# Kernel tuning notes

Hardware: AMD Instinct MI355X
Metric: run time of the kernel (lower is better)

The kernel has to match this reference:

```python
import jax, jax.numpy as jnp
import numpy as np

P, M, DG, F, H, DH = 2000, 150, 2000, 256, 4, 64
N1, N2 = P + M, P + DG          # adj1 nodes (patient+med), adj2 nodes (patient+diag)
E1, E2, EGP, EGM = 137600, 256000, 64000, 4800
GNN_LAYERS = 2
SA_HID = 128


def setup_inputs() -> dict:
    key = jax.random.key(0)
    ks = jax.random.split(key, 32)
    ri = lambda k, n, hi: jax.random.randint(k, (n,), 0, hi, dtype=jnp.int32)
    rn = lambda k, shape, scale: (jax.random.normal(k, shape, dtype=jnp.float32) * scale)
    inp = {
        'adj1_rows': ri(ks[0], E1, N1), 'adj1_cols': ri(ks[1], E1, N1),
        'adj1_vals': jax.random.uniform(ks[2], (E1,), dtype=jnp.float32),
        'adj2_rows': ri(ks[3], E2, N2), 'adj2_cols': ri(ks[4], E2, N2),
        'adj2_vals': jax.random.uniform(ks[5], (E2,), dtype=jnp.float32),
        'g0_src': ri(ks[6], EGP, P), 'g0_dst': ri(ks[7], EGP, P),
        'g1_src': ri(ks[8], EGP, P), 'g1_dst': ri(ks[9], EGP, P),
        'g2_src': ri(ks[10], EGM, M), 'g2_dst': ri(ks[11], EGM, M),
        'g3_src': ri(ks[12], EGM, M), 'g3_dst': ri(ks[13], EGM, M),
        'keepRate': 1,
        # learned parameters (xavier-ish scales)
        'pEmbed': rn(ks[14], (P, F), 0.05),
        'mEmbed': rn(ks[15], (M, F), 0.05),
        'dEmbed': rn(ks[16], (DG, F), 0.05),
        'gat_W': rn(ks[17], (4, F, H * DH), (2.0 / (F + H * DH)) ** 0.5),
        'gat_al': rn(ks[18], (4, H, DH), 0.1),
        'gat_ar': rn(ks[19], (4, H, DH), 0.1),
        'gat_b': jnp.zeros((4, H * DH), dtype=jnp.float32),
        'sa_W1': rn(ks[20], (H * DH, SA_HID), (2.0 / (H * DH + SA_HID)) ** 0.5),
        'sa_b1': jnp.zeros((SA_HID,), dtype=jnp.float32),
        'sa_W2': rn(ks[21], (SA_HID, 1), 0.1),
        'out_W': rn(ks[22], (2 * F, M), (2.0 / (2 * F + M)) ** 0.5),
        'out_b': jnp.zeros((M,), dtype=jnp.float32),
    }
    return inp


def _spmm(rows, cols, vals, x, n):
    # sparse adj @ x via gather + segment_sum
    return jax.ops.segment_sum(vals[:, None] * x[cols], rows, num_segments=n)


def _seg_softmax(e, seg, n):
    m = jax.ops.segment_max(e, seg, num_segments=n)          # [n, H]
    ex = jnp.exp(e - m[seg])
    s = jax.ops.segment_sum(ex, seg, num_segments=n)
    return ex / (s[seg] + 1e-9)


def _gat(h, W, al, ar, b, src, dst, n):
    # DGL GATConv, feat/attn dropout = 0, negative_slope = 0.2, activation = elu
    feat = (h @ W).reshape(n, H, DH)                          # [n, H, DH]
    el = (feat * al[None]).sum(-1)                            # [n, H]
    er = (feat * ar[None]).sum(-1)
    e = jax.nn.leaky_relu(el[src] + er[dst], negative_slope=0.2)  # [E, H]
    alpha = _seg_softmax(e, dst, n)                           # softmax over in-edges per dst
    out = jax.ops.segment_sum(alpha[:, :, None] * feat[src], dst, num_segments=n)
    out = out + b.reshape(1, H, DH)
    return jax.nn.elu(out).reshape(n, H * DH)


def _sem_att(z, W1, b1, W2):
    # z: [N, K, F]; shared projection; beta over K meta-paths
    w = (jnp.tanh(z @ W1 + b1) @ W2).mean(0)                  # [K, 1]
    beta = jax.nn.softmax(w, axis=0)                          # [K, 1]
    return (beta[None] * z).sum(1)                            # [N, F]


def reference(adj1_rows, adj1_cols, adj1_vals, adj2_rows, adj2_cols, adj2_vals,
              g0_src, g0_dst, g1_src, g1_dst, g2_src, g2_dst, g3_src, g3_dst,
              keepRate, pEmbed, mEmbed, dEmbed, gat_W, gat_al, gat_ar, gat_b,
              sa_W1, sa_b1, sa_W2, out_W, out_b):
    embeds1 = jnp.concatenate([pEmbed, mEmbed], axis=0)       # [N1, F]
    embeds2 = jnp.concatenate([pEmbed, dEmbed], axis=0)       # [N2, F]
    lat1, lat2 = embeds1, embeds2
    acc1 = jnp.zeros_like(embeds1)
    acc2 = jnp.zeros_like(embeds2)
    for _ in range(GNN_LAYERS):
        lat1 = jax.nn.leaky_relu(_spmm(adj1_rows, adj1_cols, adj1_vals, lat1, N1), negative_slope=0.5)
        lat2 = jax.nn.leaky_relu(_spmm(adj2_rows, adj2_cols, adj2_vals, lat2, N2), negative_slope=0.5)
        acc1 = acc1 + lat1
        acc2 = acc2 + lat2
    p1, m_gcn = acc1[:P], acc1[P:]
    p2, d_gcn = acc2[:P], acc2[P:]

    e0 = _gat(p1, gat_W[0], gat_al[0], gat_ar[0], gat_b[0], g0_src, g0_dst, P)
    e1 = _gat(p2, gat_W[1], gat_al[1], gat_ar[1], gat_b[1], g1_src, g1_dst, P)
    e2 = _gat(m_gcn, gat_W[2], gat_al[2], gat_ar[2], gat_b[2], g2_src, g2_dst, M)
    e3 = _gat(m_gcn, gat_W[3], gat_al[3], gat_ar[3], gat_b[3], g3_src, g3_dst, M)

    patient = _sem_att(jnp.stack([e0, e1], axis=1), sa_W1, sa_b1, sa_W2)  # [P, F]
    med = _sem_att(jnp.stack([e2, e3], axis=1), sa_W1, sa_b1, sa_W2)      # [M, F]

    # broadcasted pairwise concat -> ReLU -> Linear -> sum over pairing axis
    pm = jnp.concatenate([
        jnp.broadcast_to(patient[:, None, :], (P, M, F)),
        jnp.broadcast_to(med[None, :, :], (P, M, F)),
    ], axis=-1).reshape(P * M, 2 * F)
    simi = (jax.nn.relu(pm) @ out_W + out_b).reshape(P, M, M)
    simi_pm = simi.sum(axis=1)                                # [P, M]
    return (simi_pm, d_gcn, med, m_gcn, patient)
```

## Files before the change

### kernel.cpp

```cpp
#include <hip/hip_runtime.h>
#include <cmath>
#include <cstdint>

constexpr int P  = 2000, M = 150, DG = 2000, F = 256, H = 4, DH = 64;
constexpr int N1 = P + M;
constexpr int N2 = P + DG;
constexpr int E1 = 137600, E2 = 256000, EGP = 64000, EGM = 4800;
constexpr int SA_HID = 128;

constexpr int HO1 = E1, HO2 = E1 + E2, HO3 = HO2 + EGP, HO4 = HO3 + EGP,
              HO5 = HO4 + EGM, HOE = HO5 + EGM;

constexpr int CAP_A = 160;
constexpr int CAP_G = 96;
constexpr int OVF_CAP = 4096;

constexpr int CPAD = 16;

__global__ __launch_bounds__(256) void k_build(
    const int* __restrict__ a1r, const int* __restrict__ a1c, const float* __restrict__ a1v,
    const int* __restrict__ a2r, const int* __restrict__ a2c, const float* __restrict__ a2v,
    const int* __restrict__ d0, const int* __restrict__ s0,
    const int* __restrict__ d1, const int* __restrict__ s1,
    const int* __restrict__ d2, const int* __restrict__ s2,
    const int* __restrict__ d3, const int* __restrict__ s3,
    int* cur1, uint2* ell1, int* cur2, uint2* ell2,
    int* cu0, unsigned* eg0, int* cu1, unsigned* eg1,
    int* cu2, unsigned* eg2, int* cu3, unsigned* eg3,
    int* __restrict__ ovf_n, int4* __restrict__ ovf) {
  int tid = blockIdx.x * 256 + threadIdx.x;
  int T = gridDim.x * 256;
  int seg[4], row[4]; unsigned p0[4], p1[4];
#pragma unroll
  for (int u = 0; u < 4; ++u) {
    int i = tid + u * T;
    seg[u] = -1;
    if (i < HOE) {
      if (i < HO1)      { seg[u] = 0; row[u] = a1r[i]; p0[u] = (unsigned)a1c[i]; p1[u] = __float_as_uint(a1v[i]); }
      else if (i < HO2) { int j = i - HO1; seg[u] = 1; row[u] = a2r[j]; p0[u] = (unsigned)a2c[j]; p1[u] = __float_as_uint(a2v[j]); }
      else if (i < HO3) { int j = i - HO2; seg[u] = 2; row[u] = d0[j]; p0[u] = (unsigned)s0[j]; }
      else if (i < HO4) { int j = i - HO3; seg[u] = 3; row[u] = d1[j]; p0[u] = (unsigned)s1[j]; }
      else if (i < HO5) { int j = i - HO4; seg[u] = 4; row[u] = d2[j]; p0[u] = (unsigned)s2[j]; }
      else              { int j = i - HO5; seg[u] = 5; row[u] = d3[j]; p0[u] = (unsigned)s3[j]; }
    }
  }
#pragma unroll
  for (int u = 0; u < 4; ++u) {
    int r = row[u];
    switch (seg[u]) {
      case 0: { int slot = atomicAdd(&cur1[(size_t)r * CPAD], 1);
        if (slot < CAP_A) ell1[(size_t)r * CAP_A + slot] = make_uint2(p0[u], p1[u]);
        else { int o = atomicAdd(&ovf_n[0], 1); if (o < OVF_CAP) ovf[0 * OVF_CAP + o] = make_int4(r, (int)p0[u], (int)p1[u], 0); } } break;
      case 1: { int slot = atomicAdd(&cur2[(size_t)r * CPAD], 1);
        if (slot < CAP_A) ell2[(size_t)r * CAP_A + slot] = make_uint2(p0[u], p1[u]);
        else { int o = atomicAdd(&ovf_n[1], 1); if (o < OVF_CAP) ovf[1 * OVF_CAP + o] = make_int4(r, (int)p0[u], (int)p1[u], 0); } } break;
      case 2: { int slot = atomicAdd(&cu0[(size_t)r * CPAD], 1);
        if (slot < CAP_G) eg0[(size_t)r * CAP_G + slot] = p0[u];
        else { int o = atomicAdd(&ovf_n[2], 1); if (o < OVF_CAP) ovf[2 * OVF_CAP + o] = make_int4(r, (int)p0[u], 0, 0); } } break;
      case 3: { int slot = atomicAdd(&cu1[(size_t)r * CPAD], 1);
        if (slot < CAP_G) eg1[(size_t)r * CAP_G + slot] = p0[u];
        else { int o = atomicAdd(&ovf_n[3], 1); if (o < OVF_CAP) ovf[3 * OVF_CAP + o] = make_int4(r, (int)p0[u], 0, 0); } } break;
      case 4: { int slot = atomicAdd(&cu2[(size_t)r * CPAD], 1);
        if (slot < CAP_G) eg2[(size_t)r * CAP_G + slot] = p0[u];
        else { int o = atomicAdd(&ovf_n[4], 1); if (o < OVF_CAP) ovf[4 * OVF_CAP + o] = make_int4(r, (int)p0[u], 0, 0); } } break;
      case 5: { int slot = atomicAdd(&cu3[(size_t)r * CPAD], 1);
        if (slot < CAP_G) eg3[(size_t)r * CAP_G + slot] = p0[u];
        else { int o = atomicAdd(&ovf_n[5], 1); if (o < OVF_CAP) ovf[5 * OVF_CAP + o] = make_int4(r, (int)p0[u], 0, 0); } } break;
      default: break;
    }
  }
}

template<int LAYER>
__global__ __launch_bounds__(256) void k_spmm(
    const int* __restrict__ cur1, const uint2* __restrict__ ell1,
    const int* __restrict__ cur2, const uint2* __restrict__ ell2,
    const int* __restrict__ ovf_n, const int4* __restrict__ ovf,
    const float* __restrict__ pE, const float* __restrict__ mE, const float* __restrict__ dE,
    float* __restrict__ lat1, float* __restrict__ lat2,
    float* __restrict__ acc1, float* __restrict__ acc2,
    float* __restrict__ out_mgcn, float* __restrict__ out_dgcn) {
  int gw = (blockIdx.x * 256 + threadIdx.x) >> 6;
  if (gw >= N1 + N2) return;
  int lane = threadIdx.x & 63;
  bool g2 = gw >= N1;
  int row = g2 ? gw - N1 : gw;
  const uint2* pe = (g2 ? ell2 : ell1) + (size_t)row * CAP_A;
  const float* latin = g2 ? lat2 : lat1;
  const float* tailE = g2 ? dE : mE;
  int deg = (g2 ? cur2 : cur1)[(size_t)row * CPAD];
  int dn = deg < CAP_A ? deg : CAP_A;
  int fo = lane << 2;
  float4 s = {0.f, 0.f, 0.f, 0.f};
  auto fetch = [&](int c) -> float4 {
    const float* b;
    if (LAYER == 1) b = (c < P) ? (pE + (size_t)c * F) : (tailE + (size_t)(c - P) * F);
    else            b = latin + (size_t)c * F;
    return *(const float4*)(b + fo);
  };
  int i = 0;
  for (; i + 8 <= dn; i += 8) {
    uint2 m[8]; float4 a[8];
#pragma unroll
    for (int u = 0; u < 8; ++u) m[u] = pe[i + u];
#pragma unroll
    for (int u = 0; u < 8; ++u) a[u] = fetch((int)m[u].x);
#pragma unroll
    for (int u = 0; u < 8; ++u) {
      float v = __uint_as_float(m[u].y);
      s.x += v * a[u].x; s.y += v * a[u].y; s.z += v * a[u].z; s.w += v * a[u].w;
    }
  }
  for (; i + 4 <= dn; i += 4) {
    uint2 m0 = pe[i], m1 = pe[i + 1], m2 = pe[i + 2], m3 = pe[i + 3];
    float v0 = __uint_as_float(m0.y), v1 = __uint_as_float(m1.y),
          v2 = __uint_as_float(m2.y), v3 = __uint_as_float(m3.y);
    float4 a0 = fetch((int)m0.x), a1 = fetch((int)m1.x),
           a2 = fetch((int)m2.x), a3 = fetch((int)m3.x);
    s.x += v0 * a0.x + v1 * a1.x + v2 * a2.x + v3 * a3.x;
    s.y += v0 * a0.y + v1 * a1.y + v2 * a2.y + v3 * a3.y;
    s.z += v0 * a0.z + v1 * a1.z + v2 * a2.z + v3 * a3.z;
    s.w += v0 * a0.w + v1 * a1.w + v2 * a2.w + v3 * a3.w;
  }
  for (; i < dn; ++i) {
    uint2 m = pe[i];
    float v = __uint_as_float(m.y);
    float4 a = fetch((int)m.x);
    s.x += v * a.x; s.y += v * a.y; s.z += v * a.z; s.w += v * a.w;
  }
  {
    int gi = g2 ? 1 : 0;
    int on = ovf_n[gi];
    if (on > 0) {
      const int4* ol = ovf + gi * OVF_CAP;
      for (int k = 0; k < on; ++k) {
        int4 e = ol[k];
        if (e.x == row) {
          float v = __int_as_float(e.z);
          float4 a = fetch(e.y);
          s.x += v * a.x; s.y += v * a.y; s.z += v * a.z; s.w += v * a.w;
        }
      }
    }
  }
  float4 l;
  l.x = s.x > 0.f ? s.x : 0.5f * s.x;
  l.y = s.y > 0.f ? s.y : 0.5f * s.y;
  l.z = s.z > 0.f ? s.z : 0.5f * s.z;
  l.w = s.w > 0.f ? s.w : 0.5f * s.w;
  if (LAYER == 1) {
    *(float4*)((g2 ? lat2 : lat1) + (size_t)row * F + fo) = l;
  } else {
    float4 b = *(const float4*)(latin + (size_t)row * F + fo);
    float4 a = {b.x + l.x, b.y + l.y, b.z + l.z, b.w + l.w};
    *(float4*)((g2 ? acc2 : acc1) + (size_t)row * F + fo) = a;
    if (row >= P)
      *(float4*)((g2 ? out_dgcn : out_mgcn) + (size_t)(row - P) * F + fo) = a;
  }
}

constexpr int FR  = 8;
constexpr int NB0 = (P + FR - 1) / FR;
constexpr int NB2 = (M + FR - 1) / FR;
constexpr int FEAT_BLOCKS = 2 * NB0 + 2 * NB2;

__global__ __launch_bounds__(256) void k_gat_feat_all(
    const float* __restrict__ acc1, const float* __restrict__ acc2,
    const float* __restrict__ gat_W, const float* __restrict__ gat_al,
    const float* __restrict__ gat_ar,
    float* __restrict__ f0, float* __restrict__ f1,
    float* __restrict__ f2, float* __restrict__ f3,
    float* __restrict__ el, float* __restrict__ er) {
  int b = blockIdx.x;
  int g, rb, n; const float* h; float* fout;
  if (b < NB0)            { g = 0; rb = b;              n = P; h = acc1; fout = f0; }
  else if (b < 2 * NB0)   { g = 1; rb = b - NB0;        n = P; h = acc2; fout = f1; }
  else if (b < 2*NB0+NB2) { g = 2; rb = b - 2 * NB0;    n = M; h = acc1 + (size_t)P * F; fout = f2; }
  else                    { g = 3; rb = b - 2*NB0 - NB2; n = M; h = acc1 + (size_t)P * F; fout = f3; }
  int elo = (g == 0) ? 0 : (g == 1) ? P * H : (g == 2) ? 2 * P * H : (2 * P + M) * H;
  const float* W = gat_W + (size_t)g * F * F;
  __shared__ float hs[FR][F];
  int t = threadIdx.x;
  int r0 = rb * FR;
  for (int q = t; q < FR * 64; q += 256) {
    int r = q >> 6, ln = q & 63;
    int row = r0 + r;
    float4 v = {0.f, 0.f, 0.f, 0.f};
    if (row < n) v = *(const float4*)(h + (size_t)row * F + (ln << 2));
    *(float4*)&hs[r][ln << 2] = v;
  }
  __syncthreads();
  float acc[FR];
#pragma unroll
  for (int r = 0; r < FR; ++r) acc[r] = 0.f;
  for (int k = 0; k < F; k += 4) {
    float w0 = W[(size_t)k * F + t],       w1 = W[(size_t)(k + 1) * F + t],
          w2 = W[(size_t)(k + 2) * F + t], w3 = W[(size_t)(k + 3) * F + t];
#pragma unroll
    for (int r = 0; r < FR; ++r) {
      float4 h4 = *(const float4*)&hs[r][k];
      acc[r] += h4.x * w0 + h4.y * w1 + h4.z * w2 + h4.w * w3;
    }
  }
  int head = t >> 6, d = t & 63;
  float av = gat_al[g * H * DH + head * DH + d];
  float rv = gat_ar[g * H * DH + head * DH + d];
#pragma unroll
  for (int r = 0; r < FR; ++r) {
    int row = r0 + r;
    if (row < n) {
      fout[(size_t)row * F + t] = acc[r];
      float cl = acc[r] * av, cr = acc[r] * rv;
      for (int o = 32; o > 0; o >>= 1) {
        cl += __shfl_down(cl, o, 64);
        cr += __shfl_down(cr, o, 64);
      }
      if (d == 0) { el[elo + row * H + head] = cl; er[elo + row * H + head] = cr; }
    }
  }
}

__global__ __launch_bounds__(256) void k_gat_agg_all(
    const int* __restrict__ cu0, const unsigned* __restrict__ eg0,
    const int* __restrict__ cu1, const unsigned* __restrict__ eg1,
    const int* __restrict__ cu2, const unsigned* __restrict__ eg2,
    const int* __restrict__ cu3, const unsigned* __restrict__ eg3,
    const int* __restrict__ ovf_n, const int4* __restrict__ ovf,
    const float* __restrict__ el, const float* __restrict__ er,
    const float* __restrict__ f0, const float* __restrict__ f1,
    const float* __restrict__ f2, const float* __restrict__ f3,
    const float* __restrict__ gat_b,
    float* __restrict__ e0, float* __restrict__ e1,
    float* __restrict__ e2, float* __restrict__ e3) {
  int gw = (blockIdx.x * 256 + threadIdx.x) >> 6;
  if (gw >= 2 * P + 2 * M) return;
  int lane = threadIdx.x & 63;
  int g, row; const int* cu; const unsigned* eg; const float* feat; float* out; int elo;
  if (gw < P)            { g = 0; row = gw;             cu = cu0; eg = eg0; feat = f0; out = e0; elo = 0; }
  else if (gw < 2 * P)   { g = 1; row = gw - P;         cu = cu1; eg = eg1; feat = f1; out = e1; elo = P * H; }
  else if (gw < 2*P + M) { g = 2; row = gw - 2 * P;     cu = cu2; eg = eg2; feat = f2; out = e2; elo = 2 * P * H; }
  else                   { g = 3; row = gw - 2 * P - M; cu = cu3; eg = eg3; feat = f3; out = e3; elo = (2 * P + M) * H; }
  int head = lane >> 4;
  int fo = lane << 2;
  const float* elb = el + elo;
  float erv = er[elo + row * H + head];
  int deg = cu[(size_t)row * CPAD];
  int dn = deg < CAP_G ? deg : CAP_G;
  const unsigned* ps = eg + (size_t)row * CAP_G;
  int on = ovf_n[2 + g];
  const int4* ol = ovf + (2 + g) * OVF_CAP;
  float mx = -3.4e38f;
  int i = 0;
  for (; i + 4 <= dn; i += 4) {
    int s0 = (int)ps[i], s1 = (int)ps[i + 1], s2 = (int)ps[i + 2], s3 = (int)ps[i + 3];
    float a = elb[s0 * H + head] + erv, b = elb[s1 * H + head] + erv,
          c = elb[s2 * H + head] + erv, d = elb[s3 * H + head] + erv;
    a = a > 0.f ? a : 0.2f * a; b = b > 0.f ? b : 0.2f * b;
    c = c > 0.f ? c : 0.2f * c; d = d > 0.f ? d : 0.2f * d;
    mx = fmaxf(mx, fmaxf(fmaxf(a, b), fmaxf(c, d)));
  }
  for (; i < dn; ++i) {
    float a = elb[(int)ps[i] * H + head] + erv;
    a = a > 0.f ? a : 0.2f * a;
    mx = fmaxf(mx, a);
  }
  if (on > 0) {
    for (int k = 0; k < on; ++k) {
      int4 e = ol[k];
      if (e.x == row) {
        float a = elb[e.y * H + head] + erv;
        a = a > 0.f ? a : 0.2f * a;
        mx = fmaxf(mx, a);
      }
    }
  }
  float ssum = 0.f;
  float4 acc = {0.f, 0.f, 0.f, 0.f};
  i = 0;
  for (; i + 2 <= dn; i += 2) {
    int s0 = (int)ps[i], s1 = (int)ps[i + 1];
    float a = elb[s0 * H + head] + erv; a = a > 0.f ? a : 0.2f * a;
    float b = elb[s1 * H + head] + erv; b = b > 0.f ? b : 0.2f * b;
    float x0 = expf(a - mx), x1 = expf(b - mx);
    float4 q0 = *(const float4*)(feat + (size_t)s0 * F + fo);
    float4 q1 = *(const float4*)(feat + (size_t)s1 * F + fo);
    ssum += x0 + x1;
    acc.x += x0 * q0.x + x1 * q1.x;
    acc.y += x0 * q0.y + x1 * q1.y;
    acc.z += x0 * q0.z + x1 * q1.z;
    acc.w += x0 * q0.w + x1 * q1.w;
  }
  for (; i < dn; ++i) {
    int s0 = (int)ps[i];
    float a = elb[s0 * H + head] + erv; a = a > 0.f ? a : 0.2f * a;
    float x0 = expf(a - mx);
    float4 q0 = *(const float4*)(feat + (size_t)s0 * F + fo);
    ssum += x0;
    acc.x += x0 * q0.x; acc.y += x0 * q0.y; acc.z += x0 * q0.z; acc.w += x0 * q0.w;
  }
  if (on > 0) {
    for (int k = 0; k < on; ++k) {
      int4 e = ol[k];
      if (e.x == row) {
        float a = elb[e.y * H + head] + erv; a = a > 0.f ? a : 0.2f * a;
        float x0 = expf(a - mx);
        float4 q0 = *(const float4*)(feat + (size_t)e.y * F + fo);
        ssum += x0;
        acc.x += x0 * q0.x; acc.y += x0 * q0.y; acc.z += x0 * q0.z; acc.w += x0 * q0.w;
      }
    }
  }
  float inv = 1.f / (ssum + 1e-9f);
  const float* bb = gat_b + g * F + fo;
  float4 v = {acc.x * inv + bb[0], acc.y * inv + bb[1],
              acc.z * inv + bb[2], acc.w * inv + bb[3]};
  v.x = v.x > 0.f ? v.x : expm1f(v.x);
  v.y = v.y > 0.f ? v.y : expm1f(v.y);
  v.z = v.z > 0.f ? v.z : expm1f(v.z);
  v.w = v.w > 0.f ? v.w : expm1f(v.w);
  *(float4*)(out + (size_t)row * F + fo) = v;
}

constexpr int SR  = 8;
constexpr int SB0 = (P + SR - 1) / SR;
constexpr int SB2 = (M + SR - 1) / SR;
constexpr int SEM_BLOCKS = 2 * SB0 + 2 * SB2;

__global__ __launch_bounds__(128) void k_sem_w_all(
    const float* __restrict__ e0, const float* __restrict__ e1,
    const float* __restrict__ e2, const float* __restrict__ e3,
    const float* __restrict__ W1, const float* __restrict__ b1,
    const float* __restrict__ W2, float* __restrict__ w) {
  int b = blockIdx.x;
  int zid, rb, n; const float* z;
  if (b < SB0)            { zid = 0; rb = b;             n = P; z = e0; }
  else if (b < 2 * SB0)   { zid = 1; rb = b - SB0;       n = P; z = e1; }
  else if (b < 2*SB0+SB2) { zid = 2; rb = b - 2 * SB0;   n = M; z = e2; }
  else                    { zid = 3; rb = b - 2*SB0-SB2; n = M; z = e3; }
  __shared__ float zs[SR][F];
  int t = threadIdx.x;
  int r0 = rb * SR;
  for (int q = t; q < SR * 64; q += 128) {
    int r = q >> 6, ln = q & 63;
    int row = r0 + r;
    float4 v = {0.f, 0.f, 0.f, 0.f};
    if (row < n) v = *(const float4*)(z + (size_t)row * F + (ln << 2));
    *(float4*)&zs[r][ln << 2] = v;
  }
  __syncthreads();
  float hid[SR];
#pragma unroll
  for (int r = 0; r < SR; ++r) hid[r] = b1[t];
  for (int k = 0; k < F; k += 4) {
    float w0 = W1[(size_t)k * SA_HID + t],       w1 = W1[(size_t)(k + 1) * SA_HID + t],
          w2 = W1[(size_t)(k + 2) * SA_HID + t], w3 = W1[(size_t)(k + 3) * SA_HID + t];
#pragma unroll
    for (int r = 0; r < SR; ++r) {
      float4 z4 = *(const float4*)&zs[r][k];
      hid[r] += z4.x * w0 + z4.y * w1 + z4.z * w2 + z4.w * w3;
    }
  }
  float w2v = W2[t];
  float local = 0.f;
  for (int r = 0; r < SR; ++r) {
    int row = r0 + r;
    if (row < n) local += tanhf(hid[r]) * w2v;
  }
  for (int o = 32; o > 0; o >>= 1) local += __shfl_down(local, o, 64);
  __shared__ float pp[2];
  if ((t & 63) == 0) pp[t >> 6] = local;
  __syncthreads();
  if (t == 0) atomicAdd(&w[zid], pp[0] + pp[1]);
}

__global__ __launch_bounds__(256) void k_med_cvec(
    const float* __restrict__ e2, const float* __restrict__ e3,
    const float* __restrict__ w, const float* __restrict__ outW,
    const float* __restrict__ outb,
    float* __restrict__ out_med, float* __restrict__ cbuf) {
  int t = threadIdx.x;
  float m0 = w[2] * (1.f / M), m1 = w[3] * (1.f / M);
  float mxv = fmaxf(m0, m1);
  float a0 = expf(m0 - mxv), a1 = expf(m1 - mxv);
  float sc = 1.f / (a0 + a1);
  a0 *= sc; a1 *= sc;
  float4 rs = {0.f, 0.f, 0.f, 0.f};
  for (int j = t; j < M * F / 4; j += 256) {
    float4 u0 = ((const float4*)e2)[j], u1 = ((const float4*)e3)[j];
    float4 r = {a0 * u0.x + a1 * u1.x, a0 * u0.y + a1 * u1.y,
                a0 * u0.z + a1 * u1.z, a0 * u0.w + a1 * u1.w};
    ((float4*)out_med)[j] = r;
    rs.x += r.x > 0.f ? r.x : 0.f;
    rs.y += r.y > 0.f ? r.y : 0.f;
    rs.z += r.z > 0.f ? r.z : 0.f;
    rs.w += r.w > 0.f ? r.w : 0.f;
  }
  __shared__ float4 sv4[4][64];
  sv4[t >> 6][t & 63] = rs;
  __syncthreads();
  __shared__ float sv[F];
  if (t < 64) {
    float4 a = sv4[0][t], b = sv4[1][t], c = sv4[2][t], d = sv4[3][t];
    sv[t * 4 + 0] = a.x + b.x + c.x + d.x;
    sv[t * 4 + 1] = a.y + b.y + c.y + d.y;
    sv[t * 4 + 2] = a.z + b.z + c.z + d.z;
    sv[t * 4 + 3] = a.w + b.w + c.w + d.w;
  }
  __syncthreads();
  if (t < M) {
    float cc = (float)M * outb[t];
    for (int f = 0; f < F; f += 4) {
      cc += sv[f]     * outW[(size_t)(F + f) * M + t]
          + sv[f + 1] * outW[(size_t)(F + f + 1) * M + t]
          + sv[f + 2] * outW[(size_t)(F + f + 2) * M + t]
          + sv[f + 3] * outW[(size_t)(F + f + 3) * M + t];
    }
    cbuf[t] = cc;
  }
}

constexpr int FIN_R = 8;
__global__ __launch_bounds__(256) void k_final(
    const float* __restrict__ e0, const float* __restrict__ e1,
    const float* __restrict__ w, const float* __restrict__ outW,
    const float* __restrict__ c,
    float* __restrict__ out_pat, float* __restrict__ simi) {
  float m0 = w[0] * (1.f / P), m1 = w[1] * (1.f / P);
  float mxv = fmaxf(m0, m1);
  float a0 = expf(m0 - mxv), a1 = expf(m1 - mxv);
  float sc = 1.f / (a0 + a1);
  a0 *= sc; a1 *= sc;
  __shared__ float psh[FIN_R][F];
  int t = threadIdx.x;
  int r0 = blockIdx.x * FIN_R;
  for (int q = t; q < FIN_R * 64; q += 256) {
    int r = q >> 6, ln = q & 63;
    size_t off = (size_t)(r0 + r) * F + (ln << 2);
    float4 u0 = *(const float4*)(e0 + off), u1 = *(const float4*)(e1 + off);
    float4 v = {a0 * u0.x + a1 * u1.x, a0 * u0.y + a1 * u1.y,
                a0 * u0.z + a1 * u1.z, a0 * u0.w + a1 * u1.w};
    *(float4*)(out_pat + off) = v;
    v.x = v.x > 0.f ? v.x : 0.f; v.y = v.y > 0.f ? v.y : 0.f;
    v.z = v.z > 0.f ? v.z : 0.f; v.w = v.w > 0.f ? v.w : 0.f;
    *(float4*)&psh[r][ln << 2] = v;
  }
  __syncthreads();
  if (t < M) {
    float acc[FIN_R];
#pragma unroll
    for (int r = 0; r < FIN_R; ++r) acc[r] = 0.f;
    for (int f = 0; f < F; f += 4) {
      float w0 = outW[(size_t)f * M + t],       w1 = outW[(size_t)(f + 1) * M + t],
            w2 = outW[(size_t)(f + 2) * M + t], w3 = outW[(size_t)(f + 3) * M + t];
#pragma unroll
      for (int r = 0; r < FIN_R; ++r) {
        float4 p4 = *(const float4*)&psh[r][f];
        acc[r] += p4.x * w0 + p4.y * w1 + p4.z * w2 + p4.w * w3;
      }
    }
    float cv = c[t];
    for (int r = 0; r < FIN_R; ++r)
      simi[(size_t)(r0 + r) * M + t] = (float)M * acc[r] + cv;
  }
}

extern "C" void kernel_launch(void* const* d_in, const int* in_sizes, int n_in,
                              void* d_out, int out_size, void* d_ws, size_t ws_size,
                              hipStream_t stream) {
  const int*   adj1_rows = (const int*)d_in[0];
  const int*   adj1_cols = (const int*)d_in[1];
  const float* adj1_vals = (const float*)d_in[2];
  const int*   adj2_rows = (const int*)d_in[3];
  const int*   adj2_cols = (const int*)d_in[4];
  const float* adj2_vals = (const float*)d_in[5];
  const int*   g0_src = (const int*)d_in[6];
  const int*   g0_dst = (const int*)d_in[7];
  const int*   g1_src = (const int*)d_in[8];
  const int*   g1_dst = (const int*)d_in[9];
  const int*   g2_src = (const int*)d_in[10];
  const int*   g2_dst = (const int*)d_in[11];
  const int*   g3_src = (const int*)d_in[12];
  const int*   g3_dst = (const int*)d_in[13];
  const float* pE     = (const float*)d_in[15];
  const float* mE     = (const float*)d_in[16];
  const float* dE     = (const float*)d_in[17];
  const float* gat_W  = (const float*)d_in[18];
  const float* gat_al = (const float*)d_in[19];
  const float* gat_ar = (const float*)d_in[20];
  const float* gat_b  = (const float*)d_in[21];
  const float* sa_W1  = (const float*)d_in[22];
  const float* sa_b1  = (const float*)d_in[23];
  const float* sa_W2  = (const float*)d_in[24];
  const float* out_W  = (const float*)d_in[25];
  const float* out_b  = (const float*)d_in[26];

  int* ip = (int*)d_ws;
  int* cur1 = ip; ip += (size_t)N1 * CPAD;
  int* cur2 = ip; ip += (size_t)N2 * CPAD;
  int* cu0  = ip; ip += (size_t)P * CPAD;
  int* cu1  = ip; ip += (size_t)P * CPAD;
  int* cu2  = ip; ip += (size_t)M * CPAD;
  int* cu3  = ip; ip += (size_t)M * CPAD;
  int* ovf_n = ip; ip += 6;
  float* wbuf = (float*)ip; ip += 4;
  size_t memset_bytes = (size_t)((char*)ip - (char*)d_ws);

  uintptr_t up = ((uintptr_t)ip + 15) & ~(uintptr_t)15;
  int4* ovf = (int4*)up;
  uint2* ell1 = (uint2*)(ovf + 6 * OVF_CAP);
  uint2* ell2 = ell1 + (size_t)N1 * CAP_A;
  unsigned* eg0 = (unsigned*)(ell2 + (size_t)N2 * CAP_A);
  unsigned* eg1 = eg0 + (size_t)P * CAP_G;
  unsigned* eg2 = eg1 + (size_t)P * CAP_G;
  unsigned* eg3 = eg2 + (size_t)M * CAP_G;
  float* fp = (float*)(eg3 + (size_t)M * CAP_G);
  float* lat1 = fp; fp += (size_t)N1 * F;
  float* lat2 = fp; fp += (size_t)N2 * F;
  float* acc1 = fp; fp += (size_t)N1 * F;
  float* acc2 = fp; fp += (size_t)N2 * F;
  float* f0   = fp; fp += (size_t)P * F;
  float* f1   = fp; fp += (size_t)P * F;
  float* f2   = fp; fp += (size_t)M * F;
  float* f3   = fp; fp += (size_t)M * F;
  float* el   = fp; fp += (size_t)(2 * P + 2 * M) * H;
  float* er   = fp; fp += (size_t)(2 * P + 2 * M) * H;
  float* e0b  = fp; fp += (size_t)P * F;
  float* e1b  = fp; fp += (size_t)P * F;
  float* e2b  = fp; fp += (size_t)M * F;
  float* e3b  = fp; fp += (size_t)M * F;
  float* cbuf = fp; fp += 256;

  float* out_simi = (float*)d_out;
  float* out_dgcn = out_simi + (size_t)P * M;
  float* out_med  = out_dgcn + (size_t)DG * F;
  float* out_mgcn = out_med  + (size_t)M * F;
  float* out_pat  = out_mgcn + (size_t)M * F;

  hipMemsetAsync(d_ws, 0, memset_bytes, stream);

  int eb = ((HOE + 3) / 4 + 255) / 256;
  k_build<<<eb, 256, 0, stream>>>(adj1_rows, adj1_cols, adj1_vals,
                                  adj2_rows, adj2_cols, adj2_vals,
                                  g0_dst, g0_src, g1_dst, g1_src,
                                  g2_dst, g2_src, g3_dst, g3_src,
                                  cur1, ell1, cur2, ell2,
                                  cu0, eg0, cu1, eg1, cu2, eg2, cu3, eg3,
                                  ovf_n, ovf);

  int sb = ((N1 + N2) * 64 + 255) / 256;
  k_spmm<1><<<sb, 256, 0, stream>>>(cur1, ell1, cur2, ell2, ovf_n, ovf, pE, mE, dE,
                                    lat1, lat2, acc1, acc2, out_mgcn, out_dgcn);
  k_spmm<2><<<sb, 256, 0, stream>>>(cur1, ell1, cur2, ell2, ovf_n, ovf, pE, mE, dE,
                                    lat1, lat2, acc1, acc2, out_mgcn, out_dgcn);

  k_gat_feat_all<<<FEAT_BLOCKS, 256, 0, stream>>>(acc1, acc2, gat_W, gat_al, gat_ar,
                                                  f0, f1, f2, f3, el, er);
  int ab = ((2 * P + 2 * M) * 64 + 255) / 256;
  k_gat_agg_all<<<ab, 256, 0, stream>>>(cu0, eg0, cu1, eg1, cu2, eg2, cu3, eg3,
                                        ovf_n, ovf, el, er, f0, f1, f2, f3, gat_b,
                                        e0b, e1b, e2b, e3b);

  k_sem_w_all<<<SEM_BLOCKS, 128, 0, stream>>>(e0b, e1b, e2b, e3b, sa_W1, sa_b1, sa_W2, wbuf);

  k_med_cvec<<<1, 256, 0, stream>>>(e2b, e3b, wbuf, out_W, out_b, out_med, cbuf);

  k_final<<<P / FIN_R, 256, 0, stream>>>(e0b, e1b, wbuf, out_W, cbuf, out_pat, out_simi);
}
```

Baseline: 313.4 us.

## Store gathered features in fp16 for SpMM and GAT aggregation

Embeddings are cast to half precision inside the build kernel. Layer-1 SpMM now also writes a half-precision copy of its output, and the GAT feature projections are stored as half. Both SpMM layers and the GAT aggregation then gather half rows and convert them to fp32 for accumulation, which halves the bytes moved by these random gathers. Row-block sizes for the feature and semantic-attention kernels are also doubled. The cost is an extra cast pass and extra stores, plus reduced precision in the gathered operands that may affect accuracy.

```diff
diff --git a/kernel.cpp b/kernel.cpp
--- a/kernel.cpp
+++ b/kernel.cpp
@@ -1,4 +1,5 @@
 #include <hip/hip_runtime.h>
+#include <hip/hip_fp16.h>
 #include <cmath>
 #include <cstdint>
 
@@ -16,6 +17,22 @@
 constexpr int OVF_CAP = 4096;
 
 constexpr int CPAD = 16;
+
+__device__ __forceinline__ float4 h4_to_f4(const __half* p) {
+  union { ushort4 u4; __half2 h2[2]; } u;
+  u.u4 = *(const ushort4*)p;
+  float2 lo = __half22float2(u.h2[0]);
+  float2 hi = __half22float2(u.h2[1]);
+  return make_float4(lo.x, lo.y, hi.x, hi.y);
+}
+__device__ __forceinline__ void f4_to_h4(__half* p, float4 v) {
+  union { ushort4 u4; __half2 h2[2]; } u;
+  u.h2[0] = __float22half2_rn(make_float2(v.x, v.y));
+  u.h2[1] = __float22half2_rn(make_float2(v.z, v.w));
+  *(ushort4*)p = u.u4;
+}
+
+constexpr int CAST_CH = (P * F + M * F + DG * F) / 8;
 
 __global__ __launch_bounds__(256) void k_build(
     const int* __restrict__ a1r, const int* __restrict__ a1c, const float* __restrict__ a1v,
@@ -27,7 +44,10 @@
     int* cur1, uint2* ell1, int* cur2, uint2* ell2,
     int* cu0, unsigned* eg0, int* cu1, unsigned* eg1,
     int* cu2, unsigned* eg2, int* cu3, unsigned* eg3,
-    int* __restrict__ ovf_n, int4* __restrict__ ovf) {
+    int* __restrict__ ovf_n, int4* __restrict__ ovf,
+    const float* __restrict__ pEf, const float* __restrict__ mEf,
+    const float* __restrict__ dEf,
+    __half* __restrict__ pEh, __half* __restrict__ mEh, __half* __restrict__ dEh) {
   int tid = blockIdx.x * 256 + threadIdx.x;
   int T = gridDim.x * 256;
   int seg[4], row[4]; unsigned p0[4], p1[4];
@@ -69,6 +89,16 @@
       default: break;
     }
   }
+  for (int c = tid; c < CAST_CH; c += T) {
+    int j = c * 8;
+    const float* src; __half* dst;
+    if (j < P * F)              { src = pEf + j;               dst = pEh + j; }
+    else if (j < P * F + M * F) { src = mEf + (j - P * F);     dst = mEh + (j - P * F); }
+    else                        { src = dEf + (j - P*F - M*F); dst = dEh + (j - P*F - M*F); }
+    float4 a = *(const float4*)src, b = *(const float4*)(src + 4);
+    f4_to_h4(dst, a);
+    f4_to_h4(dst + 4, b);
+  }
 }
 
 template<int LAYER>
@@ -76,8 +106,10 @@
     const int* __restrict__ cur1, const uint2* __restrict__ ell1,
     const int* __restrict__ cur2, const uint2* __restrict__ ell2,
     const int* __restrict__ ovf_n, const int4* __restrict__ ovf,
-    const float* __restrict__ pE, const float* __restrict__ mE, const float* __restrict__ dE,
-    float* __restrict__ lat1, float* __restrict__ lat2,
+    const __half* __restrict__ pEh, const __half* __restrict__ mEh,
+    const __half* __restrict__ dEh,
+    float* __restrict__ lat1f, float* __restrict__ lat2f,
+    __half* __restrict__ lat1h, __half* __restrict__ lat2h,
     float* __restrict__ acc1, float* __restrict__ acc2,
     float* __restrict__ out_mgcn, float* __restrict__ out_dgcn) {
   int gw = (blockIdx.x * 256 + threadIdx.x) >> 6;
@@ -86,17 +118,17 @@
   bool g2 = gw >= N1;
   int row = g2 ? gw - N1 : gw;
   const uint2* pe = (g2 ? ell2 : ell1) + (size_t)row * CAP_A;
-  const float* latin = g2 ? lat2 : lat1;
-  const float* tailE = g2 ? dE : mE;
+  const __half* latinh = g2 ? lat2h : lat1h;
+  const __half* tailEh = g2 ? dEh : mEh;
   int deg = (g2 ? cur2 : cur1)[(size_t)row * CPAD];
   int dn = deg < CAP_A ? deg : CAP_A;
   int fo = lane << 2;
   float4 s = {0.f, 0.f, 0.f, 0.f};
   auto fetch = [&](int c) -> float4 {
-    const float* b;
-    if (LAYER == 1) b = (c < P) ? (pE + (size_t)c * F) : (tailE + (size_t)(c - P) * F);
-    else            b = latin + (size_t)c * F;
-    return *(const float4*)(b + fo);
+    const __half* b;
+    if (LAYER == 1) b = (c < P) ? (pEh + (size_t)c * F) : (tailEh + (size_t)(c - P) * F);
+    else            b = latinh + (size_t)c * F;
+    return h4_to_f4(b + fo);
   };
   int i = 0;
   for (; i + 8 <= dn; i += 8) {
@@ -149,9 +181,11 @@
   l.z = s.z > 0.f ? s.z : 0.5f * s.z;
   l.w = s.w > 0.f ? s.w : 0.5f * s.w;
   if (LAYER == 1) {
-    *(float4*)((g2 ? lat2 : lat1) + (size_t)row * F + fo) = l;
+    *(float4*)((g2 ? lat2f : lat1f) + (size_t)row * F + fo) = l;
+    f4_to_h4((g2 ? lat2h : lat1h) + (size_t)row * F + fo, l);
   } else {
-    float4 b = *(const float4*)(latin + (size_t)row * F + fo);
+    const float* latf = g2 ? lat2f : lat1f;
+    float4 b = *(const float4*)(latf + (size_t)row * F + fo);
     float4 a = {b.x + l.x, b.y + l.y, b.z + l.z, b.w + l.w};
     *(float4*)((g2 ? acc2 : acc1) + (size_t)row * F + fo) = a;
     if (row >= P)
@@ -159,7 +193,7 @@
   }
 }
 
-constexpr int FR  = 8;
+constexpr int FR  = 16;
 constexpr int NB0 = (P + FR - 1) / FR;
 constexpr int NB2 = (M + FR - 1) / FR;
 constexpr int FEAT_BLOCKS = 2 * NB0 + 2 * NB2;
@@ -168,11 +202,11 @@
     const float* __restrict__ acc1, const float* __restrict__ acc2,
     const float* __restrict__ gat_W, const float* __restrict__ gat_al,
     const float* __restrict__ gat_ar,
-    float* __restrict__ f0, float* __restrict__ f1,
-    float* __restrict__ f2, float* __restrict__ f3,
+    __half* __restrict__ f0, __half* __restrict__ f1,
+    __half* __restrict__ f2, __half* __restrict__ f3,
     float* __restrict__ el, float* __restrict__ er) {
   int b = blockIdx.x;
-  int g, rb, n; const float* h; float* fout;
+  int g, rb, n; const float* h; __half* fout;
   if (b < NB0)            { g = 0; rb = b;              n = P; h = acc1; fout = f0; }
   else if (b < 2 * NB0)   { g = 1; rb = b - NB0;        n = P; h = acc2; fout = f1; }
   else if (b < 2*NB0+NB2) { g = 2; rb = b - 2 * NB0;    n = M; h = acc1 + (size_t)P * F; fout = f2; }
@@ -209,7 +243,7 @@
   for (int r = 0; r < FR; ++r) {
     int row = r0 + r;
     if (row < n) {
-      fout[(size_t)row * F + t] = acc[r];
+      fout[(size_t)row * F + t] = __float2half_rn(acc[r]);
       float cl = acc[r] * av, cr = acc[r] * rv;
       for (int o = 32; o > 0; o >>= 1) {
         cl += __shfl_down(cl, o, 64);
@@ -227,15 +261,15 @@
     const int* __restrict__ cu3, const unsigned* __restrict__ eg3,
     const int* __restrict__ ovf_n, const int4* __restrict__ ovf,
     const float* __restrict__ el, const float* __restrict__ er,
-    const float* __restrict__ f0, const float* __restrict__ f1,
-    const float* __restrict__ f2, const float* __restrict__ f3,
+    const __half* __restrict__ f0, const __half* __restrict__ f1,
+    const __half* __restrict__ f2, const __half* __restrict__ f3,
     const float* __restrict__ gat_b,
     float* __restrict__ e0, float* __restrict__ e1,
     float* __restrict__ e2, float* __restrict__ e3) {
   int gw = (blockIdx.x * 256 + threadIdx.x) >> 6;
   if (gw >= 2 * P + 2 * M) return;
   int lane = threadIdx.x & 63;
-  int g, row; const int* cu; const unsigned* eg; const float* feat; float* out; int elo;
+  int g, row; const int* cu; const unsigned* eg; const __half* feat; float* out; int elo;
   if (gw < P)            { g = 0; row = gw;             cu = cu0; eg = eg0; feat = f0; out = e0; elo = 0; }
   else if (gw < 2 * P)   { g = 1; row = gw - P;         cu = cu1; eg = eg1; feat = f1; out = e1; elo = P * H; }
   else if (gw < 2*P + M) { g = 2; row = gw - 2 * P;     cu = cu2; eg = eg2; feat = f2; out = e2; elo = 2 * P * H; }
@@ -282,8 +316,8 @@
     float a = elb[s0 * H + head] + erv; a = a > 0.f ? a : 0.2f * a;
     float b = elb[s1 * H + head] + erv; b = b > 0.f ? b : 0.2f * b;
     float x0 = expf(a - mx), x1 = expf(b - mx);
-    float4 q0 = *(const float4*)(feat + (size_t)s0 * F + fo);
-    float4 q1 = *(const float4*)(feat + (size_t)s1 * F + fo);
+    float4 q0 = h4_to_f4(feat + (size_t)s0 * F + fo);
+    float4 q1 = h4_to_f4(feat + (size_t)s1 * F + fo);
     ssum += x0 + x1;
     acc.x += x0 * q0.x + x1 * q1.x;
     acc.y += x0 * q0.y + x1 * q1.y;
@@ -294,7 +328,7 @@
     int s0 = (int)ps[i];
     float a = elb[s0 * H + head] + erv; a = a > 0.f ? a : 0.2f * a;
     float x0 = expf(a - mx);
-    float4 q0 = *(const float4*)(feat + (size_t)s0 * F + fo);
+    float4 q0 = h4_to_f4(feat + (size_t)s0 * F + fo);
     ssum += x0;
     acc.x += x0 * q0.x; acc.y += x0 * q0.y; acc.z += x0 * q0.z; acc.w += x0 * q0.w;
   }
@@ -304,7 +338,7 @@
       if (e.x == row) {
         float a = elb[e.y * H + head] + erv; a = a > 0.f ? a : 0.2f * a;
         float x0 = expf(a - mx);
-        float4 q0 = *(const float4*)(feat + (size_t)e.y * F + fo);
+        float4 q0 = h4_to_f4(feat + (size_t)e.y * F + fo);
         ssum += x0;
         acc.x += x0 * q0.x; acc.y += x0 * q0.y; acc.z += x0 * q0.z; acc.w += x0 * q0.w;
       }
@@ -321,7 +355,7 @@
   *(float4*)(out + (size_t)row * F + fo) = v;
 }
 
-constexpr int SR  = 8;
+constexpr int SR  = 16;
 constexpr int SB0 = (P + SR - 1) / SR;
 constexpr int SB2 = (M + SR - 1) / SR;
 constexpr int SEM_BLOCKS = 2 * SB0 + 2 * SB2;
@@ -513,22 +547,28 @@
   unsigned* eg1 = eg0 + (size_t)P * CAP_G;
   unsigned* eg2 = eg1 + (size_t)P * CAP_G;
   unsigned* eg3 = eg2 + (size_t)M * CAP_G;
-  float* fp = (float*)(eg3 + (size_t)M * CAP_G);
-  float* lat1 = fp; fp += (size_t)N1 * F;
-  float* lat2 = fp; fp += (size_t)N2 * F;
-  float* acc1 = fp; fp += (size_t)N1 * F;
-  float* acc2 = fp; fp += (size_t)N2 * F;
-  float* f0   = fp; fp += (size_t)P * F;
-  float* f1   = fp; fp += (size_t)P * F;
-  float* f2   = fp; fp += (size_t)M * F;
-  float* f3   = fp; fp += (size_t)M * F;
-  float* el   = fp; fp += (size_t)(2 * P + 2 * M) * H;
-  float* er   = fp; fp += (size_t)(2 * P + 2 * M) * H;
-  float* e0b  = fp; fp += (size_t)P * F;
-  float* e1b  = fp; fp += (size_t)P * F;
-  float* e2b  = fp; fp += (size_t)M * F;
-  float* e3b  = fp; fp += (size_t)M * F;
-  float* cbuf = fp; fp += 256;
+  __half* hp = (__half*)(eg3 + (size_t)M * CAP_G);
+  __half* pEh   = hp; hp += (size_t)P * F;
+  __half* mEh   = hp; hp += (size_t)M * F;
+  __half* dEh   = hp; hp += (size_t)DG * F;
+  __half* lat1h = hp; hp += (size_t)N1 * F;
+  __half* lat2h = hp; hp += (size_t)N2 * F;
+  __half* f0h   = hp; hp += (size_t)P * F;
+  __half* f1h   = hp; hp += (size_t)P * F;
+  __half* f2h   = hp; hp += (size_t)M * F;
+  __half* f3h   = hp; hp += (size_t)M * F;
+  float* fp = (float*)hp;
+  float* lat1f = fp; fp += (size_t)N1 * F;
+  float* lat2f = fp; fp += (size_t)N2 * F;
+  float* acc1  = fp; fp += (size_t)N1 * F;
+  float* acc2  = fp; fp += (size_t)N2 * F;
+  float* el    = fp; fp += (size_t)(2 * P + 2 * M) * H;
+  float* er    = fp; fp += (size_t)(2 * P + 2 * M) * H;
+  float* e0b   = fp; fp += (size_t)P * F;
+  float* e1b   = fp; fp += (size_t)P * F;
+  float* e2b   = fp; fp += (size_t)M * F;
+  float* e3b   = fp; fp += (size_t)M * F;
+  float* cbuf  = fp; fp += 256;
 
   float* out_simi = (float*)d_out;
   float* out_dgcn = out_simi + (size_t)P * M;
@@ -545,19 +585,22 @@
                                   g2_dst, g2_src, g3_dst, g3_src,
                                   cur1, ell1, cur2, ell2,
                                   cu0, eg0, cu1, eg1, cu2, eg2, cu3, eg3,
-                                  ovf_n, ovf);
+                                  ovf_n, ovf,
+                                  pE, mE, dE, pEh, mEh, dEh);
 
   int sb = ((N1 + N2) * 64 + 255) / 256;
-  k_spmm<1><<<sb, 256, 0, stream>>>(cur1, ell1, cur2, ell2, ovf_n, ovf, pE, mE, dE,
-                                    lat1, lat2, acc1, acc2, out_mgcn, out_dgcn);
-  k_spmm<2><<<sb, 256, 0, stream>>>(cur1, ell1, cur2, ell2, ovf_n, ovf, pE, mE, dE,
-                                    lat1, lat2, acc1, acc2, out_mgcn, out_dgcn);
+  k_spmm<1><<<sb, 256, 0, stream>>>(cur1, ell1, cur2, ell2, ovf_n, ovf,
+                                    pEh, mEh, dEh, lat1f, lat2f, lat1h, lat2h,
+                                    acc1, acc2, out_mgcn, out_dgcn);
+  k_spmm<2><<<sb, 256, 0, stream>>>(cur1, ell1, cur2, ell2, ovf_n, ovf,
+                                    pEh, mEh, dEh, lat1f, lat2f, lat1h, lat2h,
+                                    acc1, acc2, out_mgcn, out_dgcn);
 
   k_gat_feat_all<<<FEAT_BLOCKS, 256, 0, stream>>>(acc1, acc2, gat_W, gat_al, gat_ar,
-                                                  f0, f1, f2, f3, el, er);
+                                                  f0h, f1h, f2h, f3h, el, er);
   int ab = ((2 * P + 2 * M) * 64 + 255) / 256;
   k_gat_agg_all<<<ab, 256, 0, stream>>>(cu0, eg0, cu1, eg1, cu2, eg2, cu3, eg3,
-                                        ovf_n, ovf, el, er, f0, f1, f2, f3, gat_b,
+                                        ovf_n, ovf, el, er, f0h, f1h, f2h, f3h, gat_b,
                                         e0b, e1b, e2b, e3b);
 
   k_sem_w_all<<<SEM_BLOCKS, 128, 0, stream>>>(e0b, e1b, e2b, e3b, sa_W1, sa_b1, sa_W2, wbuf);
```

After: 319.6 us. No clear change (+2.0%).
